# Kernel optimization log

Measured on AMD Instinct MI355X. Metric: run time of the kernel, lower is better.

## Reference

```python
import jax, jax.numpy as jnp
import numpy as np

NEG_SLOPE = 0.2  # PyG GATConv default LeakyReLU slope
EPS = 1e-16


def gat_conv(x, src, dst, W, att_src, att_dst, bias, concat):
    """One GATConv layer (PyG semantics, self-loops already in src/dst).
    x: [N, Fin]; src/dst: [E'] int; W: [Fin, H*C]; att_*: [H, C]; bias: [H*C] or [C].
    """
    N = x.shape[0]
    H, C = att_src.shape
    h = (x @ W).reshape(N, H, C)                      # [N, H, C]
    a_s = jnp.einsum('nhc,hc->nh', h, att_src)        # [N, H]
    a_d = jnp.einsum('nhc,hc->nh', h, att_dst)        # [N, H]
    logits = jax.nn.leaky_relu(a_s[src] + a_d[dst], NEG_SLOPE)  # [E', H]
    # segment softmax over incoming edges of each destination node
    m = jax.ops.segment_max(logits, dst, num_segments=N)        # [N, H]
    m = jnp.where(jnp.isfinite(m), m, 0.0)
    e = jnp.exp(logits - m[dst])                                # [E', H]
    denom = jax.ops.segment_sum(e, dst, num_segments=N)         # [N, H]
    alpha = e / (denom[dst] + EPS)                              # [E', H]
    msg = h[src] * alpha[:, :, None]                            # [E', H, C]
    out = jax.ops.segment_sum(msg, dst, num_segments=N)         # [N, H, C]
    out = out.reshape(N, H * C) if concat else out.mean(axis=1)
    return out + bias


def setup_inputs() -> dict:
    key = jax.random.key(0)
    ks = jax.random.split(key, 8)
    N, E, IN, HID, OUT, H1 = 50000, 800000, 128, 64, 32, 2
    x = jax.random.normal(ks[0], (N, IN), dtype=jnp.float32)
    edge_index = jax.random.randint(ks[1], (2, E), 0, N, dtype=jnp.int32)
    # glorot-ish scaled params
    W1 = jax.random.normal(ks[2], (IN, H1 * HID), dtype=jnp.float32) * (1.0 / np.sqrt(IN))
    att_src1 = jax.random.normal(ks[3], (H1, HID), dtype=jnp.float32) * (1.0 / np.sqrt(HID))
    att_dst1 = jax.random.normal(ks[4], (H1, HID), dtype=jnp.float32) * (1.0 / np.sqrt(HID))
    bias1 = jnp.zeros((H1 * HID,), dtype=jnp.float32)
    W2 = jax.random.normal(ks[5], (H1 * HID, OUT), dtype=jnp.float32) * (1.0 / np.sqrt(H1 * HID))
    att_src2 = jax.random.normal(ks[6], (1, OUT), dtype=jnp.float32) * (1.0 / np.sqrt(OUT))
    att_dst2 = jax.random.normal(ks[7], (1, OUT), dtype=jnp.float32) * (1.0 / np.sqrt(OUT))
    bias2 = jnp.zeros((OUT,), dtype=jnp.float32)
    return {"x": x, "edge_index": edge_index, "W1": W1, "att_src1": att_src1,
            "att_dst1": att_dst1, "bias1": bias1, "W2": W2, "att_src2": att_src2,
            "att_dst2": att_dst2, "bias2": bias2}


def reference(x, edge_index, W1, att_src1, att_dst1, bias1, W2, att_src2, att_dst2, bias2):
    N = x.shape[0]
    loops = jnp.arange(N, dtype=edge_index.dtype)
    src = jnp.concatenate([edge_index[0], loops])   # add self loops (PyG default)
    dst = jnp.concatenate([edge_index[1], loops])
    h = gat_conv(x, src, dst, W1, att_src1, att_dst1, bias1, concat=True)
    h = jax.nn.relu(h)
    out = gat_conv(h, src, dst, W2, att_src2, att_dst2, bias2, concat=False)
    return out
```

## Files before the change

kernel.cpp:

```cpp
#include <hip/hip_runtime.h>
#include <math.h>


typedef __bf16 bf16x8 __attribute__((ext_vector_type(8)));
typedef float f32x4 __attribute__((ext_vector_type(4)));

__device__ __forceinline__ float lrelu(float x) { return x > 0.f ? x : 0.2f * x; }

__device__ __forceinline__ unsigned short f2bf(float x) {
  unsigned u = __float_as_uint(x);
  return (unsigned short)((u + 0x7fffu + ((u >> 16) & 1u)) >> 16);
}
__device__ __forceinline__ float2 bf2_unpack(unsigned u) {
  return make_float2(__uint_as_float(u << 16), __uint_as_float(u & 0xffff0000u));
}
__device__ __forceinline__ float readlane_f(float v, int l) {
  return __uint_as_float((unsigned)__builtin_amdgcn_readlane(__float_as_uint(v), l));
}

constexpr int CAP = 5632;

__launch_bounds__(512)
__global__ void k_partition(const int* __restrict__ srcA, const int* __restrict__ dstA,
                            int E, int Nn, int* __restrict__ gcnt,
                            unsigned* __restrict__ bkt) {
  __shared__ int hist[256];
  __shared__ int bbase[256];
  const int NBK = (Nn + 255) >> 8;
  const int tid = threadIdx.x;
  for (int i = tid; i < 256; i += 512) hist[i] = 0;
  __syncthreads();
  const int tot = E + Nn;
  const int g0 = blockIdx.x * 4096;
  unsigned pk[8]; int bk[8], rk[8]; int cnt = 0;
#pragma unroll
  for (int j = 0; j < 8; ++j) {
    int g = g0 + j * 512 + tid;
    if (g >= tot) break;
    int s, d;
    if (g < E) { s = srcA[g]; d = dstA[g]; } else { s = g - E; d = s; }
    int b = d >> 8;
    pk[cnt] = (unsigned)s | ((unsigned)(d & 255) << 16);
    bk[cnt] = b;
    rk[cnt] = atomicAdd(&hist[b], 1);
    cnt++;
  }
  __syncthreads();
  for (int i = tid; i < 256; i += 512) {
    int h = (i < NBK) ? hist[i] : 0;
    bbase[i] = h ? atomicAdd(&gcnt[i], h) : 0;
  }
  __syncthreads();
  for (int j = 0; j < cnt; ++j) {
    int pos = bbase[bk[j]] + rk[j];
    if (pos < CAP) bkt[(size_t)bk[j] * CAP + pos] = pk[j];
  }
}

__launch_bounds__(512)
__global__ void k_fine(const unsigned* __restrict__ bkt, const int* __restrict__ gcnt,
                       int Nn, int tot, int* __restrict__ offs, unsigned* __restrict__ csr) {
  __shared__ int fc[256];
  __shared__ int lo[256];
  __shared__ int cur[256];
  __shared__ int baseS;
  const int b = blockIdx.x;
  const int tid = threadIdx.x;
  int m = gcnt[b]; if (m > CAP) m = CAP;
  const unsigned* p = bkt + (size_t)b * CAP;
  if (b == 0 && tid == 0) offs[Nn] = tot;
  for (int i = tid; i < 256; i += 512) fc[i] = 0;
  __syncthreads();
  for (int i = tid; i < m; i += 512) atomicAdd(&fc[p[i] >> 16], 1);
  __syncthreads();
  if (tid < 64) {
    int s = 0;
    for (int c = tid; c < b; c += 64) s += gcnt[c];
#pragma unroll
    for (int o = 32; o; o >>= 1) s += __shfl_xor(s, o);
    if (tid == 0) baseS = s;
    int carry = 0;
    for (int c = 0; c < 256; c += 64) {
      int v = fc[c + tid]; int x = v;
#pragma unroll
      for (int o = 1; o < 64; o <<= 1) { int t = __shfl_up(x, o); if (tid >= o) x += t; }
      lo[c + tid] = carry + x - v;
      carry += __shfl(x, 63);
    }
  }
  __syncthreads();
  const int base = baseS;
  for (int i = tid; i < 256; i += 512) {
    cur[i] = lo[i];
    int n = (b << 8) + i;
    if (n < Nn) offs[n] = base + lo[i];
  }
  __syncthreads();
  const unsigned hi = ((unsigned)b) << 24;
  for (int i = tid; i < m; i += 512) {
    unsigned e = p[i];
    int pos = atomicAdd(&cur[e >> 16], 1);
    csr[base + pos] = hi | ((e >> 16) << 16) | (e & 0xffffu);
  }
}

__launch_bounds__(256)
__global__ void k_gemm1(const float* __restrict__ A, const float* __restrict__ B,
                        unsigned short* __restrict__ Cb,
                        const float* __restrict__ attS, const float* __restrict__ attD,
                        float* __restrict__ asO, float* __restrict__ adO, int M) {
  __shared__ union { unsigned short bl[32 * 64 * 8]; float accl[64 * 132]; } sm;
  const int tid = threadIdx.x;
  const int lane = tid & 63, w = tid >> 6;
  const int row0 = blockIdx.x * 64;
  for (int i = tid; i < 128 * 32; i += 256) {
    int k = i >> 5, n4 = (i & 31) << 2;
    float4 v = *(const float4*)(B + k * 128 + n4);
    int c = k >> 5, q = (k >> 3) & 3, j = k & 7;
    float vv[4] = {v.x, v.y, v.z, v.w};
#pragma unroll
    for (int u2 = 0; u2 < 4; ++u2) {
      int n = n4 + u2, t = n >> 4, l = q * 16 + (n & 15);
      sm.bl[((t * 4 + c) * 64 + l) * 8 + j] = f2bf(vv[u2]);
    }
  }
  int mrow = row0 + 16 * w + (lane & 15);
  bool rok = mrow < M;
  const int q = lane >> 4;
  bf16x8 afr[4];
  union { unsigned short s[8]; bf16x8 b; } cv;
#pragma unroll
  for (int c = 0; c < 4; ++c) {
    float4 u0 = make_float4(0.f, 0.f, 0.f, 0.f), u1 = u0;
    if (rok) {
      const float* ap = A + (size_t)mrow * 128 + c * 32 + q * 8;
      u0 = *(const float4*)ap; u1 = *(const float4*)(ap + 4);
    }
    cv.s[0] = f2bf(u0.x); cv.s[1] = f2bf(u0.y); cv.s[2] = f2bf(u0.z); cv.s[3] = f2bf(u0.w);
    cv.s[4] = f2bf(u1.x); cv.s[5] = f2bf(u1.y); cv.s[6] = f2bf(u1.z); cv.s[7] = f2bf(u1.w);
    afr[c] = cv.b;
  }
  __syncthreads();
  f32x4 acc[8];
#pragma unroll
  for (int t = 0; t < 8; ++t) {
    f32x4 a = {0.f, 0.f, 0.f, 0.f};
#pragma unroll
    for (int c = 0; c < 4; ++c) {
      bf16x8 bf = *(((const bf16x8*)sm.bl) + (t * 4 + c) * 64 + lane);
      a = __builtin_amdgcn_mfma_f32_16x16x32_bf16(afr[c], bf, a, 0, 0, 0);
    }
    acc[t] = a;
  }
  __syncthreads();
  {
    int rbase = 16 * w + q * 4, cl = lane & 15;
#pragma unroll
    for (int t = 0; t < 8; ++t)
#pragma unroll
      for (int r = 0; r < 4; ++r)
        sm.accl[(rbase + r) * 132 + 16 * t + cl] = acc[t][r];
  }
  __syncthreads();
  {
    int row = tid >> 2, cg = tid & 3, c0 = cg * 32;
    int grow = row0 + row;
    const float* ar = &sm.accl[row * 132 + c0];
    float ps = 0.f, pd = 0.f;
    unsigned pkv[16];
#pragma unroll
    for (int u2 = 0; u2 < 8; ++u2) {
      float4 v  = *(const float4*)(ar + u2 * 4);
      float4 s4 = *(const float4*)(attS + c0 + u2 * 4);
      float4 d4 = *(const float4*)(attD + c0 + u2 * 4);
      ps += v.x * s4.x + v.y * s4.y + v.z * s4.z + v.w * s4.w;
      pd += v.x * d4.x + v.y * d4.y + v.z * d4.z + v.w * d4.w;
      pkv[u2 * 2]     = (unsigned)f2bf(v.x) | ((unsigned)f2bf(v.y) << 16);
      pkv[u2 * 2 + 1] = (unsigned)f2bf(v.z) | ((unsigned)f2bf(v.w) << 16);
    }
    ps += __shfl_xor(ps, 1); pd += __shfl_xor(pd, 1);
    if (grow < M) {
      if ((tid & 1) == 0) {
        int head = (tid >> 1) & 1;
        asO[(size_t)grow * 2 + head] = ps; adO[(size_t)grow * 2 + head] = pd;
      }
      unsigned* cp = (unsigned*)(Cb + (size_t)grow * 128 + c0);
      *(uint4*)(cp)      = make_uint4(pkv[0], pkv[1], pkv[2], pkv[3]);
      *(uint4*)(cp + 4)  = make_uint4(pkv[4], pkv[5], pkv[6], pkv[7]);
      *(uint4*)(cp + 8)  = make_uint4(pkv[8], pkv[9], pkv[10], pkv[11]);
      *(uint4*)(cp + 12) = make_uint4(pkv[12], pkv[13], pkv[14], pkv[15]);
    }
  }
}

__launch_bounds__(256)
__global__ void k_gemm2(const unsigned* __restrict__ Ab, const float* __restrict__ B,
                        unsigned short* __restrict__ Cb,
                        const float* __restrict__ attS, const float* __restrict__ attD,
                        float* __restrict__ asO, float* __restrict__ adO, int M) {
  __shared__ unsigned short bl[8 * 64 * 8];
  __shared__ float accl[64 * 36];
  const int tid = threadIdx.x;
  const int lane = tid & 63, w = tid >> 6;
  const int row0 = blockIdx.x * 64;
  for (int i = tid; i < 128 * 8; i += 256) {
    int k = i >> 3, n4 = (i & 7) << 2;
    float4 v = *(const float4*)(B + k * 32 + n4);
    int c = k >> 5, q = (k >> 3) & 3, j = k & 7;
    float vv[4] = {v.x, v.y, v.z, v.w};
#pragma unroll
    for (int u2 = 0; u2 < 4; ++u2) {
      int n = n4 + u2, t = n >> 4, l = q * 16 + (n & 15);
      bl[((t * 4 + c) * 64 + l) * 8 + j] = f2bf(vv[u2]);
    }
  }
  int mrow = row0 + 16 * w + (lane & 15);
  bool rok = mrow < M;
  const int q = lane >> 4;
  bf16x8 afr[4];
#pragma unroll
  for (int c = 0; c < 4; ++c) {
    uint4 u = make_uint4(0u, 0u, 0u, 0u);
    if (rok) u = *(const uint4*)(Ab + (size_t)mrow * 64 + c * 16 + q * 4);
    afr[c] = __builtin_bit_cast(bf16x8, u);
  }
  __syncthreads();
  f32x4 acc[2];
#pragma unroll
  for (int t = 0; t < 2; ++t) {
    f32x4 a = {0.f, 0.f, 0.f, 0.f};
#pragma unroll
    for (int c = 0; c < 4; ++c) {
      bf16x8 bf = *(((const bf16x8*)bl) + (t * 4 + c) * 64 + lane);
      a = __builtin_amdgcn_mfma_f32_16x16x32_bf16(afr[c], bf, a, 0, 0, 0);
    }
    acc[t] = a;
  }
  {
    int rbase = 16 * w + q * 4, cl = lane & 15;
#pragma unroll
    for (int t = 0; t < 2; ++t)
#pragma unroll
      for (int r = 0; r < 4; ++r)
        accl[(rbase + r) * 36 + 16 * t + cl] = acc[t][r];
  }
  __syncthreads();
  {
    int row = tid >> 2, cg = tid & 3, c0 = cg * 8;
    int grow = row0 + row;
    const float* ar = &accl[row * 36 + c0];
    float ps = 0.f, pd = 0.f;
    unsigned pk[4];
#pragma unroll
    for (int u2 = 0; u2 < 2; ++u2) {
      float4 v  = *(const float4*)(ar + u2 * 4);
      float4 s4 = *(const float4*)(attS + c0 + u2 * 4);
      float4 d4 = *(const float4*)(attD + c0 + u2 * 4);
      ps += v.x * s4.x + v.y * s4.y + v.z * s4.z + v.w * s4.w;
      pd += v.x * d4.x + v.y * d4.y + v.z * d4.z + v.w * d4.w;
      pk[u2 * 2]     = (unsigned)f2bf(v.x) | ((unsigned)f2bf(v.y) << 16);
      pk[u2 * 2 + 1] = (unsigned)f2bf(v.z) | ((unsigned)f2bf(v.w) << 16);
    }
    ps += __shfl_xor(ps, 1); ps += __shfl_xor(ps, 2);
    pd += __shfl_xor(pd, 1); pd += __shfl_xor(pd, 2);
    if (grow < M) {
      if (cg == 0) { asO[grow] = ps; adO[grow] = pd; }
      *(uint4*)(Cb + (size_t)grow * 32 + c0) = make_uint4(pk[0], pk[1], pk[2], pk[3]);
    }
  }
}

__global__ void k_agg1(const unsigned* __restrict__ h1b, const float* __restrict__ as1,
                       const float* __restrict__ ad1, const int* __restrict__ offs,
                       const unsigned* __restrict__ csr, const float* __restrict__ bias,
                       unsigned* __restrict__ outb, int Nn) {
  int n = blockIdx.x * (blockDim.x >> 6) + (threadIdx.x >> 6);
  if (n >= Nn) return;
  int lane = threadIdx.x & 63;
  int head = lane >> 5;
  int beg = offs[n], end = offs[n + 1];
  float2 adn = ((const float2*)ad1)[n];
  float ax = 0.f, ay = 0.f, den = 0.f;
  int i = beg;
  while (i < end) {
    int m = end - i; if (m > 64) m = 64;
    int idx = i + lane;
    bool ok = idx < end;
    unsigned e = ok ? csr[idx] : 0u;
    int sv = (int)(e & 0xffffu);
    float w0 = 0.f, w1 = 0.f;
    if (ok) {
      float2 a = ((const float2*)as1)[sv];
      w0 = __expf(lrelu(a.x + adn.x));
      w1 = __expf(lrelu(a.y + adn.y));
    }
    int j = 0;
    for (; j + 4 <= m; j += 4) {
#pragma unroll
      for (int u = 0; u < 4; ++u) {
        int s = __builtin_amdgcn_readlane(sv, j + u);
        float ex = readlane_f(w0, j + u), ey = readlane_f(w1, j + u);
        float ee = head ? ey : ex;
        float2 v = bf2_unpack(h1b[(size_t)s * 64 + lane]);
        ax += ee * v.x; ay += ee * v.y; den += ee;
      }
    }
    for (; j < m; ++j) {
      int s = __builtin_amdgcn_readlane(sv, j);
      float ex = readlane_f(w0, j), ey = readlane_f(w1, j);
      float ee = head ? ey : ex;
      float2 v = bf2_unpack(h1b[(size_t)s * 64 + lane]);
      ax += ee * v.x; ay += ee * v.y; den += ee;
    }
    i += m;
  }
  float inv = 1.f / (den + 1e-16f);
  const float2 bv = ((const float2*)bias)[lane];
  float o0 = ax * inv + bv.x; o0 = o0 > 0.f ? o0 : 0.f;
  float o1 = ay * inv + bv.y; o1 = o1 > 0.f ? o1 : 0.f;
  outb[(size_t)n * 64 + lane] = (unsigned)f2bf(o0) | ((unsigned)f2bf(o1) << 16);
}

__global__ void k_agg2(const unsigned* __restrict__ h2b, const float* __restrict__ as2,
                       const float* __restrict__ ad2, const int* __restrict__ offs,
                       const unsigned* __restrict__ csr, const float* __restrict__ bias,
                       float* __restrict__ out, int Nn) {
  int n = blockIdx.x * (blockDim.x >> 6) + (threadIdx.x >> 6);
  if (n >= Nn) return;
  int lane = threadIdx.x & 63;
  int g = lane >> 4, cp = lane & 15;
  int beg = offs[n], end = offs[n + 1];
  float adn = ad2[n];
  float ax = 0.f, ay = 0.f, den = 0.f;
  int i = beg;
  while (i < end) {
    int m = end - i; if (m > 64) m = 64;
    int idx = i + lane;
    bool ok = idx < end;
    unsigned e = ok ? csr[idx] : 0u;
    int sv = (int)(e & 0xffffu);
    float wv = ok ? __expf(lrelu(as2[sv] + adn)) : 0.f;
    for (int j = 0; j < m; j += 4) {
      int jj = j + g;
      float ee = __shfl(wv, jj);
      int s = __shfl(sv, jj);
      float2 v = bf2_unpack(h2b[(size_t)s * 16 + cp]);
      ax += ee * v.x; ay += ee * v.y; den += ee;
    }
    i += m;
  }
  ax += __shfl_xor(ax, 16); ay += __shfl_xor(ay, 16); den += __shfl_xor(den, 16);
  ax += __shfl_xor(ax, 32); ay += __shfl_xor(ay, 32); den += __shfl_xor(den, 32);
  if (lane < 16) {
    float inv = 1.f / (den + 1e-16f);
    const float2 bv = ((const float2*)bias)[cp];
    ((float2*)out)[(size_t)n * 16 + cp] =
        make_float2(ax * inv + bv.x, ay * inv + bv.y);
  }
}

extern "C" void kernel_launch(void* const* d_in, const int* in_sizes, int n_in,
                              void* d_out, int out_size, void* d_ws, size_t ws_size,
                              hipStream_t stream) {
  const float* x      = (const float*)d_in[0];
  const int*   ei     = (const int*)d_in[1];
  const float* W1     = (const float*)d_in[2];
  const float* att_s1 = (const float*)d_in[3];
  const float* att_d1 = (const float*)d_in[4];
  const float* bias1  = (const float*)d_in[5];
  const float* W2     = (const float*)d_in[6];
  const float* att_s2 = (const float*)d_in[7];
  const float* att_d2 = (const float*)d_in[8];
  const float* bias2  = (const float*)d_in[9];
  float* out = (float*)d_out;

  const int N = in_sizes[0] / 128;
  const int E = in_sizes[1] / 2;
  const int* srcA = ei;
  const int* dstA = ei + E;
  const int tot = E + N;
  const int NBK = (N + 255) >> 8;

  char* w = (char*)d_ws;
  auto alloc = [&](size_t bytes) { char* p = w; w += (bytes + 255) / 256 * 256; return p; };
  unsigned short* h1b = (unsigned short*)alloc((size_t)N * 128 * 2);
  unsigned* h2in_b    = (unsigned*)alloc((size_t)N * 64 * 4);
  unsigned short* h2b = (unsigned short*)alloc((size_t)N * 32 * 2);
  float* as1    = (float*)alloc((size_t)N * 2 * 4);
  float* ad1    = (float*)alloc((size_t)N * 2 * 4);
  float* as2    = (float*)alloc((size_t)N * 4);
  float* ad2    = (float*)alloc((size_t)N * 4);
  int*   gcnt   = (int*)alloc((size_t)NBK * 4);
  unsigned* bkt = (unsigned*)alloc((size_t)NBK * CAP * 4);
  int*   offs   = (int*)alloc((size_t)(N + 1) * 4);
  unsigned* csr = (unsigned*)alloc((size_t)tot * 4);

  hipMemsetAsync(gcnt, 0, (size_t)NBK * 4, stream);
  k_partition<<<(tot + 4095) / 4096, 512, 0, stream>>>(srcA, dstA, E, N, gcnt, bkt);
  k_fine<<<NBK, 512, 0, stream>>>(bkt, gcnt, N, tot, offs, csr);

  int gb = (N + 63) / 64;
  k_gemm1<<<gb, 256, 0, stream>>>(x, W1, h1b, att_s1, att_d1, as1, ad1, N);
  int nb = (N + 3) / 4;
  k_agg1<<<nb, 256, 0, stream>>>((const unsigned*)h1b, as1, ad1, offs, csr, bias1, h2in_b, N);

  k_gemm2<<<gb, 256, 0, stream>>>(h2in_b, W2, h2b, att_s2, att_d2, as2, ad2, N);
  k_agg2<<<nb, 256, 0, stream>>>((const unsigned*)h2b, as2, ad2, offs, csr, bias2, out, N);
}
```

Measured before the change: 203.2 us.

## Fuse edge partition with first GEMM into one launch; rework agg1 per-head edge weights

The edge bucketing pass and the first-layer GEMM are merged into a single kernel whose blocks branch by index, so the two independent stages run concurrently and one launch is removed. The partition blocks drop to 256 threads, each handling 16 edges. k_agg1 now computes one exp per lane per head (32 edges per chunk, one head per half-wave) and fetches weights with ds_bpermute instead of two readlanes plus a select. The CSR entry now holds only the source index. The trade-off is a shared-memory union sized for the GEMM, which may lower occupancy for partition blocks, and smaller edge chunks in agg1.

Measured after the change: 195.6 us. -3.7%, faster.

```diff
diff --git a/kernel.cpp b/kernel.cpp
--- a/kernel.cpp
+++ b/kernel.cpp
@@ -14,46 +14,134 @@
 __device__ __forceinline__ float2 bf2_unpack(unsigned u) {
   return make_float2(__uint_as_float(u << 16), __uint_as_float(u & 0xffff0000u));
 }
-__device__ __forceinline__ float readlane_f(float v, int l) {
-  return __uint_as_float((unsigned)__builtin_amdgcn_readlane(__float_as_uint(v), l));
-}
 
 constexpr int CAP = 5632;
 
-__launch_bounds__(512)
-__global__ void k_partition(const int* __restrict__ srcA, const int* __restrict__ dstA,
-                            int E, int Nn, int* __restrict__ gcnt,
-                            unsigned* __restrict__ bkt) {
-  __shared__ int hist[256];
-  __shared__ int bbase[256];
-  const int NBK = (Nn + 255) >> 8;
+union SharedK1 {
+  struct { int hist[256]; int bbase[256]; } part;
+  union { unsigned short bl[32 * 64 * 8]; float accl[64 * 132]; } gem;
+};
+
+__launch_bounds__(256)
+__global__ void k_csr_gemm1(const int* __restrict__ srcA, const int* __restrict__ dstA,
+                            int E, int Nn, int PB, int* __restrict__ gcnt,
+                            unsigned* __restrict__ bkt,
+                            const float* __restrict__ A, const float* __restrict__ B,
+                            unsigned short* __restrict__ Cb,
+                            const float* __restrict__ attS, const float* __restrict__ attD,
+                            float* __restrict__ asO, float* __restrict__ adO, int M) {
+  __shared__ SharedK1 sm;
   const int tid = threadIdx.x;
-  for (int i = tid; i < 256; i += 512) hist[i] = 0;
-  __syncthreads();
-  const int tot = E + Nn;
-  const int g0 = blockIdx.x * 4096;
-  unsigned pk[8]; int bk[8], rk[8]; int cnt = 0;
-#pragma unroll
-  for (int j = 0; j < 8; ++j) {
-    int g = g0 + j * 512 + tid;
-    if (g >= tot) break;
-    int s, d;
-    if (g < E) { s = srcA[g]; d = dstA[g]; } else { s = g - E; d = s; }
-    int b = d >> 8;
-    pk[cnt] = (unsigned)s | ((unsigned)(d & 255) << 16);
-    bk[cnt] = b;
-    rk[cnt] = atomicAdd(&hist[b], 1);
-    cnt++;
-  }
-  __syncthreads();
-  for (int i = tid; i < 256; i += 512) {
-    int h = (i < NBK) ? hist[i] : 0;
-    bbase[i] = h ? atomicAdd(&gcnt[i], h) : 0;
-  }
-  __syncthreads();
-  for (int j = 0; j < cnt; ++j) {
-    int pos = bbase[bk[j]] + rk[j];
-    if (pos < CAP) bkt[(size_t)bk[j] * CAP + pos] = pk[j];
+  if ((int)blockIdx.x < PB) {
+    const int NBK = (Nn + 255) >> 8;
+    for (int i = tid; i < 256; i += 256) sm.part.hist[i] = 0;
+    __syncthreads();
+    const int tot = E + Nn;
+    const int g0 = blockIdx.x * 4096;
+    unsigned pk[16]; int bk[16], rk[16]; int cnt = 0;
+#pragma unroll
+    for (int j = 0; j < 16; ++j) {
+      int g = g0 + j * 256 + tid;
+      if (g >= tot) break;
+      int s, d;
+      if (g < E) { s = srcA[g]; d = dstA[g]; } else { s = g - E; d = s; }
+      int b = d >> 8;
+      pk[cnt] = (unsigned)s | ((unsigned)(d & 255) << 16);
+      bk[cnt] = b;
+      rk[cnt] = atomicAdd(&sm.part.hist[b], 1);
+      cnt++;
+    }
+    __syncthreads();
+    for (int i = tid; i < 256; i += 256) {
+      int h = (i < NBK) ? sm.part.hist[i] : 0;
+      sm.part.bbase[i] = h ? atomicAdd(&gcnt[i], h) : 0;
+    }
+    __syncthreads();
+    for (int j = 0; j < cnt; ++j) {
+      int pos = sm.part.bbase[bk[j]] + rk[j];
+      if (pos < CAP) bkt[(size_t)bk[j] * CAP + pos] = pk[j];
+    }
+    return;
+  }
+  const int lane = tid & 63, w = tid >> 6;
+  const int row0 = (blockIdx.x - PB) * 64;
+  for (int i = tid; i < 128 * 32; i += 256) {
+    int k = i >> 5, n4 = (i & 31) << 2;
+    float4 v = *(const float4*)(B + k * 128 + n4);
+    int c = k >> 5, q = (k >> 3) & 3, j = k & 7;
+    float vv[4] = {v.x, v.y, v.z, v.w};
+#pragma unroll
+    for (int u2 = 0; u2 < 4; ++u2) {
+      int n = n4 + u2, t = n >> 4, l = q * 16 + (n & 15);
+      sm.gem.bl[((t * 4 + c) * 64 + l) * 8 + j] = f2bf(vv[u2]);
+    }
+  }
+  int mrow = row0 + 16 * w + (lane & 15);
+  bool rok = mrow < M;
+  const int q = lane >> 4;
+  bf16x8 afr[4];
+  union { unsigned short s[8]; bf16x8 b; } cv;
+#pragma unroll
+  for (int c = 0; c < 4; ++c) {
+    float4 u0 = make_float4(0.f, 0.f, 0.f, 0.f), u1 = u0;
+    if (rok) {
+      const float* ap = A + (size_t)mrow * 128 + c * 32 + q * 8;
+      u0 = *(const float4*)ap; u1 = *(const float4*)(ap + 4);
+    }
+    cv.s[0] = f2bf(u0.x); cv.s[1] = f2bf(u0.y); cv.s[2] = f2bf(u0.z); cv.s[3] = f2bf(u0.w);
+    cv.s[4] = f2bf(u1.x); cv.s[5] = f2bf(u1.y); cv.s[6] = f2bf(u1.z); cv.s[7] = f2bf(u1.w);
+    afr[c] = cv.b;
+  }
+  __syncthreads();
+  f32x4 acc[8];
+#pragma unroll
+  for (int t = 0; t < 8; ++t) {
+    f32x4 a = {0.f, 0.f, 0.f, 0.f};
+#pragma unroll
+    for (int c = 0; c < 4; ++c) {
+      bf16x8 bf = *(((const bf16x8*)sm.gem.bl) + (t * 4 + c) * 64 + lane);
+      a = __builtin_amdgcn_mfma_f32_16x16x32_bf16(afr[c], bf, a, 0, 0, 0);
+    }
+    acc[t] = a;
+  }
+  __syncthreads();
+  {
+    int rbase = 16 * w + q * 4, cl = lane & 15;
+#pragma unroll
+    for (int t = 0; t < 8; ++t)
+#pragma unroll
+      for (int r = 0; r < 4; ++r)
+        sm.gem.accl[(rbase + r) * 132 + 16 * t + cl] = acc[t][r];
+  }
+  __syncthreads();
+  {
+    int row = tid >> 2, cg = tid & 3, c0 = cg * 32;
+    int grow = row0 + row;
+    const float* ar = &sm.gem.accl[row * 132 + c0];
+    float ps = 0.f, pd = 0.f;
+    unsigned pkv[16];
+#pragma unroll
+    for (int u2 = 0; u2 < 8; ++u2) {
+      float4 v  = *(const float4*)(ar + u2 * 4);
+      float4 s4 = *(const float4*)(attS + c0 + u2 * 4);
+      float4 d4 = *(const float4*)(attD + c0 + u2 * 4);
+      ps += v.x * s4.x + v.y * s4.y + v.z * s4.z + v.w * s4.w;
+      pd += v.x * d4.x + v.y * d4.y + v.z * d4.z + v.w * d4.w;
+      pkv[u2 * 2]     = (unsigned)f2bf(v.x) | ((unsigned)f2bf(v.y) << 16);
+      pkv[u2 * 2 + 1] = (unsigned)f2bf(v.z) | ((unsigned)f2bf(v.w) << 16);
+    }
+    ps += __shfl_xor(ps, 1); pd += __shfl_xor(pd, 1);
+    if (grow < M) {
+      if ((tid & 1) == 0) {
+        int head = (tid >> 1) & 1;
+        asO[(size_t)grow * 2 + head] = ps; adO[(size_t)grow * 2 + head] = pd;
+      }
+      unsigned* cp = (unsigned*)(Cb + (size_t)grow * 128 + c0);
+      *(uint4*)(cp)      = make_uint4(pkv[0], pkv[1], pkv[2], pkv[3]);
+      *(uint4*)(cp + 4)  = make_uint4(pkv[4], pkv[5], pkv[6], pkv[7]);
+      *(uint4*)(cp + 8)  = make_uint4(pkv[8], pkv[9], pkv[10], pkv[11]);
+      *(uint4*)(cp + 12) = make_uint4(pkv[12], pkv[13], pkv[14], pkv[15]);
+    }
   }
 }
 
@@ -96,101 +184,63 @@
     if (n < Nn) offs[n] = base + lo[i];
   }
   __syncthreads();
-  const unsigned hi = ((unsigned)b) << 24;
   for (int i = tid; i < m; i += 512) {
     unsigned e = p[i];
     int pos = atomicAdd(&cur[e >> 16], 1);
-    csr[base + pos] = hi | ((e >> 16) << 16) | (e & 0xffffu);
-  }
-}
-
-__launch_bounds__(256)
-__global__ void k_gemm1(const float* __restrict__ A, const float* __restrict__ B,
-                        unsigned short* __restrict__ Cb,
-                        const float* __restrict__ attS, const float* __restrict__ attD,
-                        float* __restrict__ asO, float* __restrict__ adO, int M) {
-  __shared__ union { unsigned short bl[32 * 64 * 8]; float accl[64 * 132]; } sm;
-  const int tid = threadIdx.x;
-  const int lane = tid & 63, w = tid >> 6;
-  const int row0 = blockIdx.x * 64;
-  for (int i = tid; i < 128 * 32; i += 256) {
-    int k = i >> 5, n4 = (i & 31) << 2;
-    float4 v = *(const float4*)(B + k * 128 + n4);
-    int c = k >> 5, q = (k >> 3) & 3, j = k & 7;
-    float vv[4] = {v.x, v.y, v.z, v.w};
-#pragma unroll
-    for (int u2 = 0; u2 < 4; ++u2) {
-      int n = n4 + u2, t = n >> 4, l = q * 16 + (n & 15);
-      sm.bl[((t * 4 + c) * 64 + l) * 8 + j] = f2bf(vv[u2]);
-    }
-  }
-  int mrow = row0 + 16 * w + (lane & 15);
-  bool rok = mrow < M;
-  const int q = lane >> 4;
-  bf16x8 afr[4];
-  union { unsigned short s[8]; bf16x8 b; } cv;
-#pragma unroll
-  for (int c = 0; c < 4; ++c) {
-    float4 u0 = make_float4(0.f, 0.f, 0.f, 0.f), u1 = u0;
-    if (rok) {
-      const float* ap = A + (size_t)mrow * 128 + c * 32 + q * 8;
-      u0 = *(const float4*)ap; u1 = *(const float4*)(ap + 4);
-    }
-    cv.s[0] = f2bf(u0.x); cv.s[1] = f2bf(u0.y); cv.s[2] = f2bf(u0.z); cv.s[3] = f2bf(u0.w);
-    cv.s[4] = f2bf(u1.x); cv.s[5] = f2bf(u1.y); cv.s[6] = f2bf(u1.z); cv.s[7] = f2bf(u1.w);
-    afr[c] = cv.b;
-  }
-  __syncthreads();
-  f32x4 acc[8];
-#pragma unroll
-  for (int t = 0; t < 8; ++t) {
-    f32x4 a = {0.f, 0.f, 0.f, 0.f};
-#pragma unroll
-    for (int c = 0; c < 4; ++c) {
-      bf16x8 bf = *(((const bf16x8*)sm.bl) + (t * 4 + c) * 64 + lane);
-      a = __builtin_amdgcn_mfma_f32_16x16x32_bf16(afr[c], bf, a, 0, 0, 0);
-    }
-    acc[t] = a;
-  }
-  __syncthreads();
-  {
-    int rbase = 16 * w + q * 4, cl = lane & 15;
-#pragma unroll
-    for (int t = 0; t < 8; ++t)
-#pragma unroll
-      for (int r = 0; r < 4; ++r)
-        sm.accl[(rbase + r) * 132 + 16 * t + cl] = acc[t][r];
-  }
-  __syncthreads();
-  {
-    int row = tid >> 2, cg = tid & 3, c0 = cg * 32;
-    int grow = row0 + row;
-    const float* ar = &sm.accl[row * 132 + c0];
-    float ps = 0.f, pd = 0.f;
-    unsigned pkv[16];
-#pragma unroll
-    for (int u2 = 0; u2 < 8; ++u2) {
-      float4 v  = *(const float4*)(ar + u2 * 4);
-      float4 s4 = *(const float4*)(attS + c0 + u2 * 4);
-      float4 d4 = *(const float4*)(attD + c0 + u2 * 4);
-      ps += v.x * s4.x + v.y * s4.y + v.z * s4.z + v.w * s4.w;
-      pd += v.x * d4.x + v.y * d4.y + v.z * d4.z + v.w * d4.w;
-      pkv[u2 * 2]     = (unsigned)f2bf(v.x) | ((unsigned)f2bf(v.y) << 16);
-      pkv[u2 * 2 + 1] = (unsigned)f2bf(v.z) | ((unsigned)f2bf(v.w) << 16);
-    }
-    ps += __shfl_xor(ps, 1); pd += __shfl_xor(pd, 1);
-    if (grow < M) {
-      if ((tid & 1) == 0) {
-        int head = (tid >> 1) & 1;
-        asO[(size_t)grow * 2 + head] = ps; adO[(size_t)grow * 2 + head] = pd;
+    csr[base + pos] = e & 0xffffu;
+  }
+}
+
+__global__ void k_agg1(const unsigned* __restrict__ h1b, const float* __restrict__ as1,
+                       const float* __restrict__ ad1, const int* __restrict__ offs,
+                       const unsigned* __restrict__ csr, const float* __restrict__ bias,
+                       unsigned* __restrict__ outb, int Nn) {
+  int n = blockIdx.x * (blockDim.x >> 6) + (threadIdx.x >> 6);
+  if (n >= Nn) return;
+  int lane = threadIdx.x & 63;
+  int head = lane >> 5;
+  int el = lane & 31;
+  int pbase = (lane & 32) << 2;
+  int beg = offs[n], end = offs[n + 1];
+  float2 adn = ((const float2*)ad1)[n];
+  float adh = head ? adn.y : adn.x;
+  float ax = 0.f, ay = 0.f, den = 0.f;
+  int i = beg;
+  while (i < end) {
+    int m = end - i; if (m > 32) m = 32;
+    bool ok = el < m;
+    unsigned e = ok ? csr[i + el] : 0u;
+    int sv = (int)e;
+    float wv = 0.f;
+    if (ok) {
+      float2 a = ((const float2*)as1)[sv];
+      wv = __expf(lrelu((head ? a.y : a.x) + adh));
+    }
+    int j = 0;
+    for (; j + 4 <= m; j += 4) {
+#pragma unroll
+      for (int u = 0; u < 4; ++u) {
+        int s = __builtin_amdgcn_readlane(sv, j + u);
+        float ee = __int_as_float(
+            __builtin_amdgcn_ds_bpermute(pbase + 4 * (j + u), __float_as_int(wv)));
+        float2 v = bf2_unpack(h1b[(size_t)s * 64 + lane]);
+        ax += ee * v.x; ay += ee * v.y; den += ee;
       }
-      unsigned* cp = (unsigned*)(Cb + (size_t)grow * 128 + c0);
-      *(uint4*)(cp)      = make_uint4(pkv[0], pkv[1], pkv[2], pkv[3]);
-      *(uint4*)(cp + 4)  = make_uint4(pkv[4], pkv[5], pkv[6], pkv[7]);
-      *(uint4*)(cp + 8)  = make_uint4(pkv[8], pkv[9], pkv[10], pkv[11]);
-      *(uint4*)(cp + 12) = make_uint4(pkv[12], pkv[13], pkv[14], pkv[15]);
-    }
-  }
+    }
+    for (; j < m; ++j) {
+      int s = __builtin_amdgcn_readlane(sv, j);
+      float ee = __int_as_float(
+          __builtin_amdgcn_ds_bpermute(pbase + 4 * j, __float_as_int(wv)));
+      float2 v = bf2_unpack(h1b[(size_t)s * 64 + lane]);
+      ax += ee * v.x; ay += ee * v.y; den += ee;
+    }
+    i += m;
+  }
+  float inv = 1.f / (den + 1e-16f);
+  const float2 bv = ((const float2*)bias)[lane];
+  float o0 = ax * inv + bv.x; o0 = o0 > 0.f ? o0 : 0.f;
+  float o1 = ay * inv + bv.y; o1 = o1 > 0.f ? o1 : 0.f;
+  outb[(size_t)n * 64 + lane] = (unsigned)f2bf(o0) | ((unsigned)f2bf(o1) << 16);
 }
 
 __launch_bounds__(256)
@@ -268,57 +318,6 @@
       *(uint4*)(Cb + (size_t)grow * 32 + c0) = make_uint4(pk[0], pk[1], pk[2], pk[3]);
     }
   }
-}
-
-__global__ void k_agg1(const unsigned* __restrict__ h1b, const float* __restrict__ as1,
-                       const float* __restrict__ ad1, const int* __restrict__ offs,
-                       const unsigned* __restrict__ csr, const float* __restrict__ bias,
-                       unsigned* __restrict__ outb, int Nn) {
-  int n = blockIdx.x * (blockDim.x >> 6) + (threadIdx.x >> 6);
-  if (n >= Nn) return;
-  int lane = threadIdx.x & 63;
-  int head = lane >> 5;
-  int beg = offs[n], end = offs[n + 1];
-  float2 adn = ((const float2*)ad1)[n];
-  float ax = 0.f, ay = 0.f, den = 0.f;
-  int i = beg;
-  while (i < end) {
-    int m = end - i; if (m > 64) m = 64;
-    int idx = i + lane;
-    bool ok = idx < end;
-    unsigned e = ok ? csr[idx] : 0u;
-    int sv = (int)(e & 0xffffu);
-    float w0 = 0.f, w1 = 0.f;
-    if (ok) {
-      float2 a = ((const float2*)as1)[sv];
-      w0 = __expf(lrelu(a.x + adn.x));
-      w1 = __expf(lrelu(a.y + adn.y));
-    }
-    int j = 0;
-    for (; j + 4 <= m; j += 4) {
-#pragma unroll
-      for (int u = 0; u < 4; ++u) {
-        int s = __builtin_amdgcn_readlane(sv, j + u);
-        float ex = readlane_f(w0, j + u), ey = readlane_f(w1, j + u);
-        float ee = head ? ey : ex;
-        float2 v = bf2_unpack(h1b[(size_t)s * 64 + lane]);
-        ax += ee * v.x; ay += ee * v.y; den += ee;
-      }
-    }
-    for (; j < m; ++j) {
-      int s = __builtin_amdgcn_readlane(sv, j);
-      float ex = readlane_f(w0, j), ey = readlane_f(w1, j);
-      float ee = head ? ey : ex;
-      float2 v = bf2_unpack(h1b[(size_t)s * 64 + lane]);
-      ax += ee * v.x; ay += ee * v.y; den += ee;
-    }
-    i += m;
-  }
-  float inv = 1.f / (den + 1e-16f);
-  const float2 bv = ((const float2*)bias)[lane];
-  float o0 = ax * inv + bv.x; o0 = o0 > 0.f ? o0 : 0.f;
-  float o1 = ay * inv + bv.y; o1 = o1 > 0.f ? o1 : 0.f;
-  outb[(size_t)n * 64 + lane] = (unsigned)f2bf(o0) | ((unsigned)f2bf(o1) << 16);
 }
 
 __global__ void k_agg2(const unsigned* __restrict__ h2b, const float* __restrict__ as2,
@@ -337,8 +336,7 @@
     int m = end - i; if (m > 64) m = 64;
     int idx = i + lane;
     bool ok = idx < end;
-    unsigned e = ok ? csr[idx] : 0u;
-    int sv = (int)(e & 0xffffu);
+    int sv = ok ? (int)csr[idx] : 0;
     float wv = ok ? __expf(lrelu(as2[sv] + adn)) : 0.f;
     for (int j = 0; j < m; j += 4) {
       int jj = j + g;
@@ -396,14 +394,15 @@
   unsigned* csr = (unsigned*)alloc((size_t)tot * 4);
 
   hipMemsetAsync(gcnt, 0, (size_t)NBK * 4, stream);
-  k_partition<<<(tot + 4095) / 4096, 512, 0, stream>>>(srcA, dstA, E, N, gcnt, bkt);
+
+  const int PB = (tot + 4095) / 4096;
+  const int GB = (N + 63) / 64;
+  k_csr_gemm1<<<PB + GB, 256, 0, stream>>>(srcA, dstA, E, N, PB, gcnt, bkt,
+                                           x, W1, h1b, att_s1, att_d1, as1, ad1, N);
   k_fine<<<NBK, 512, 0, stream>>>(bkt, gcnt, N, tot, offs, csr);
 
-  int gb = (N + 63) / 64;
-  k_gemm1<<<gb, 256, 0, stream>>>(x, W1, h1b, att_s1, att_d1, as1, ad1, N);
   int nb = (N + 3) / 4;
   k_agg1<<<nb, 256, 0, stream>>>((const unsigned*)h1b, as1, ad1, offs, csr, bias1, h2in_b, N);
-
-  k_gemm2<<<gb, 256, 0, stream>>>(h2in_b, W2, h2b, att_s2, att_d2, as2, ad2, N);
+  k_gemm2<<<GB, 256, 0, stream>>>(h2in_b, W2, h2b, att_s2, att_d2, as2, ad2, N);
   k_agg2<<<nb, 256, 0, stream>>>((const unsigned*)h2b, as2, ad2, offs, csr, bias2, out, N);
 }
```
